# Optimization experiments

Measured on AMD Instinct MI355X. Metric: run time of the kernel, lower is better.

Reference implementation:

```python
import jax, jax.numpy as jnp
import numpy as np

H = 4        # no_heads
C = 32       # c_hidden per head
CQ = 128     # c_q = c_k = c_v
N = 256      # pair dim / seq len
B = 1


def setup_inputs() -> dict:
    key = jax.random.key(0)
    ks = jax.random.split(key, 8)
    q_x = jax.random.normal(ks[0], (B, N, N, CQ), dtype=jnp.float32)
    kv_x = jax.random.normal(ks[1], (B, N, N, CQ), dtype=jnp.float32)
    mask_bias = jnp.zeros((B, N, 1, 1, N), dtype=jnp.float32)
    pair_bias = jax.random.normal(ks[2], (B, 1, H, N, N), dtype=jnp.float32)
    s = 1.0 / np.sqrt(CQ)
    w_q = jax.random.normal(ks[3], (H * C, CQ), dtype=jnp.float32) * s
    w_k = jax.random.normal(ks[4], (H * C, CQ), dtype=jnp.float32) * s
    w_v = jax.random.normal(ks[5], (H * C, CQ), dtype=jnp.float32) * s
    w_g = jax.random.normal(ks[6], (H * C, CQ), dtype=jnp.float32) * s
    w_o = jax.random.normal(ks[7], (CQ, H * C), dtype=jnp.float32) * s
    return {"q_x": q_x, "kv_x": kv_x, "mask_bias": mask_bias,
            "pair_bias": pair_bias, "w_q": w_q, "w_k": w_k, "w_v": w_v,
            "w_g": w_g, "w_o": w_o}


def reference(q_x, kv_x, mask_bias, pair_bias, w_q, w_k, w_v, w_g, w_o):
    # project: [B, N, Q, c] -> [B, N, H, Q, C]
    def proj(x, w):
        y = jnp.einsum('...qc,dc->...qd', x, w)            # [B,N,Q,H*C]
        y = y.reshape(*y.shape[:-1], H, C)                 # [B,N,Q,H,C]
        return jnp.swapaxes(y, -2, -3)                     # [B,N,H,Q,C]

    q = proj(q_x, w_q) / jnp.sqrt(jnp.asarray(C, q_x.dtype))
    k = proj(kv_x, w_k)
    v = proj(kv_x, w_v)

    # scores [B, N, H, Q, K] with both biases added pre-softmax
    a = jnp.einsum('...hqd,...hkd->...hqk', q, k) + mask_bias + pair_bias
    a = jax.nn.softmax(a, axis=-1)
    o = jnp.einsum('...hqk,...hkd->...hqd', a, v)          # [B,N,H,Q,C]
    o = jnp.swapaxes(o, -2, -3)                            # [B,N,Q,H,C]
    o = o.reshape(*o.shape[:-2], H * C)                    # [B,N,Q,H*C]

    g = jax.nn.sigmoid(jnp.einsum('...qc,dc->...qd', q_x, w_g))
    o = o * g
    return jnp.einsum('...qd,cd->...qc', o, w_o)           # [B,N,Q,c_q]
```

## Files before the change

### kernel.cpp

```cpp
#include <hip/hip_runtime.h>
#include <hip/hip_bf16.h>

#define H 4
#define C 32
#define CQ 128
#define NSEQ 256
#define HC 128

typedef __bf16 bf16;
typedef __bf16 bf16x8 __attribute__((ext_vector_type(8)));
typedef __bf16 bf16x4 __attribute__((ext_vector_type(4)));
typedef float f32x4 __attribute__((ext_vector_type(4)));

#define MFMA16(a, b, c) __builtin_amdgcn_mfma_f32_16x16x32_bf16(a, b, c, 0, 0, 0)

#define LOG2E 1.4426950408889634f

__global__ __launch_bounds__(256) void prep_weights(const float* __restrict__ wq,
                                                    const float* __restrict__ wk,
                                                    const float* __restrict__ wv,
                                                    const float* __restrict__ wg,
                                                    const float* __restrict__ wo,
                                                    bf16* __restrict__ dst) {
    const int m = blockIdx.y;
    const float* src = (m == 0) ? wq : (m == 1) ? wk : (m == 2) ? wv : (m == 3) ? wg : wo;
    int i = blockIdx.x * 256 + threadIdx.x;
    float4 v = ((const float4*)src)[i];
    bf16x4 b = {(bf16)v.x, (bf16)v.y, (bf16)v.z, (bf16)v.w};
    ((bf16x4*)(dst + (size_t)m * 16384))[i] = b;
}

__global__ __launch_bounds__(256) void proj_all(const float* __restrict__ qx,
                                                const float* __restrict__ kvx,
                                                const bf16* __restrict__ wbf,
                                                bf16* __restrict__ qo,
                                                bf16* __restrict__ go,
                                                bf16* __restrict__ ko,
                                                bf16* __restrict__ vo) {
    __shared__ bf16 w1s[128][136];
    __shared__ bf16 w2s[128][136];

    const int t = threadIdx.x;
    const int mode = blockIdx.y;

    const float* x = mode ? kvx : qx;
    const bf16* w1 = wbf + (mode ? 1 : 0) * 16384;
    const bf16* w2 = wbf + (mode ? 2 : 3) * 16384;
    bf16* o1 = mode ? ko : qo;
    bf16* o2 = mode ? vo : go;

    #pragma unroll
    for (int i = t; i < 2048; i += 256) {
        int row = i >> 4, col = (i & 15) * 8;
        *(bf16x8*)&w1s[row][col] = *(const bf16x8*)&w1[row * CQ + col];
        *(bf16x8*)&w2s[row][col] = *(const bf16x8*)&w2[row * CQ + col];
    }
    __syncthreads();

    const int w = t >> 6, l = t & 63, lr = l & 15, lg = l >> 4;
    const float qscale = 0.17677669529663687f * LOG2E;

    for (int it = 0; it < 4; it++) {
        const int row0 = blockIdx.x * 256 + it * 64 + w * 16;

        bf16x8 a[4];
        #pragma unroll
        for (int ks = 0; ks < 4; ks++) {
            const float* p = x + (size_t)(row0 + lr) * CQ + ks * 32 + lg * 8;
            float4 lo = *(const float4*)p;
            float4 hi = *(const float4*)(p + 4);
            a[ks] = (bf16x8){(bf16)lo.x, (bf16)lo.y, (bf16)lo.z, (bf16)lo.w,
                             (bf16)hi.x, (bf16)hi.y, (bf16)hi.z, (bf16)hi.w};
        }

        f32x4 acc1[8], acc2[8];
        #pragma unroll
        for (int nt = 0; nt < 8; nt++) { acc1[nt] = (f32x4)0.f; acc2[nt] = (f32x4)0.f; }

        #pragma unroll
        for (int nt = 0; nt < 8; nt++) {
            #pragma unroll
            for (int ks = 0; ks < 4; ks++) {
                bf16x8 b1 = *(const bf16x8*)&w1s[nt * 16 + lr][ks * 32 + lg * 8];
                acc1[nt] = MFMA16(a[ks], b1, acc1[nt]);
            }
            #pragma unroll
            for (int ks = 0; ks < 4; ks++) {
                bf16x8 b2 = *(const bf16x8*)&w2s[nt * 16 + lr][ks * 32 + lg * 8];
                acc2[nt] = MFMA16(a[ks], b2, acc2[nt]);
            }
        }

        #pragma unroll
        for (int nt = 0; nt < 8; nt++) {
            #pragma unroll
            for (int r = 0; r < 4; r++) {
                const int row = row0 + lg * 4 + r;
                const int col = nt * 16 + lr;
                float v1 = acc1[nt][r], v2 = acc2[nt][r];
                if (mode == 0) {
                    v1 *= qscale;
                    v2 = __builtin_amdgcn_rcpf(1.f + __builtin_amdgcn_exp2f(-v2 * LOG2E));
                }
                o1[(size_t)row * HC + col] = (bf16)v1;
                o2[(size_t)row * HC + col] = (bf16)v2;
            }
        }
    }
}

__global__ __launch_bounds__(256) void attn_kernel(const bf16* __restrict__ qw,
                                                   const bf16* __restrict__ kw,
                                                   const bf16* __restrict__ vw,
                                                   const bf16* __restrict__ gw,
                                                   const float* __restrict__ pair_bias,
                                                   const float* __restrict__ mask_bias,
                                                   bf16* __restrict__ ow) {
    const int wg = blockIdx.x;
    const int swz = ((wg & 7) << 9) + (wg >> 3);
    const int qc = swz & 3;
    const int n1 = (swz >> 2) & 255;
    const int h = swz >> 10;

    __shared__ bf16 klds[256][40];
    __shared__ bf16 vts[32][256];
    __shared__ bf16 ps[4][16][132];

    const int t = threadIdx.x;

    {
        const size_t base = ((size_t)n1 * NSEQ) * HC + (size_t)h * C;
        const int rr = t >> 2, cc4 = t & 3, ch = cc4 * 8;
        #pragma unroll
        for (int p = 0; p < 4; p++) {
            int row = p * 64 + rr;
            bf16x8 kv = *(const bf16x8*)&kw[base + (size_t)row * HC + ch];
            *(bf16x8*)&klds[row][ch] = kv;
            bf16x8 vv = *(const bf16x8*)&vw[base + (size_t)row * HC + ch];
            #pragma unroll
            for (int j = 0; j < 8; j++) {
                int colw = row ^ (cc4 << 4) ^ (j << 3);
                vts[ch + j][colw] = vv[j];
            }
        }
    }

    const int w = t >> 6, l = t & 63, lr = l & 15, lg = l >> 4;
    const int qbase = qc * 64 + w * 16;

    bf16x8 qf = *(const bf16x8*)&qw[((size_t)(n1 * NSEQ + qbase + lr)) * HC + h * C + lg * 8];

    const float* pb = pair_bias + (size_t)h * NSEQ * NSEQ;
    const float* mb = mask_bias + (size_t)n1 * NSEQ;

    __syncthreads();

    f32x4 s[16];
    #pragma unroll
    for (int kt = 0; kt < 16; kt++) {
        float mbk = mb[kt * 16 + lr] * LOG2E;
        #pragma unroll
        for (int r = 0; r < 4; r++)
            s[kt][r] = fmaf(pb[(size_t)(qbase + lg * 4 + r) * NSEQ + kt * 16 + lr],
                            LOG2E, mbk);
    }
    #pragma unroll
    for (int kt = 0; kt < 16; kt++) {
        bf16x8 kf = *(const bf16x8*)&klds[kt * 16 + lr][lg * 8];
        s[kt] = MFMA16(qf, kf, s[kt]);
    }

    float pinv[4];
    #pragma unroll
    for (int r = 0; r < 4; r++) {
        float mx = s[0][r];
        #pragma unroll
        for (int kt = 1; kt < 16; kt++) mx = fmaxf(mx, s[kt][r]);
        #pragma unroll
        for (int msk = 8; msk >= 1; msk >>= 1) mx = fmaxf(mx, __shfl_xor(mx, msk, 64));
        float sum = 0.f;
        #pragma unroll
        for (int kt = 0; kt < 16; kt++) {
            float e = __builtin_amdgcn_exp2f(s[kt][r] - mx);
            s[kt][r] = e;
            sum += e;
        }
        #pragma unroll
        for (int msk = 8; msk >= 1; msk >>= 1) sum += __shfl_xor(sum, msk, 64);
        pinv[r] = __builtin_amdgcn_rcpf(sum);
    }

    f32x4 o[2];
    o[0] = (f32x4)0.f;
    o[1] = (f32x4)0.f;
    #pragma unroll
    for (int hf = 0; hf < 2; hf++) {
        #pragma unroll
        for (int kt2 = 0; kt2 < 8; kt2++) {
            #pragma unroll
            for (int r = 0; r < 4; r++)
                ps[w][lg * 4 + r][kt2 * 16 + lr] = (bf16)(s[hf * 8 + kt2][r] * pinv[r]);
        }
        #pragma unroll
        for (int kh = 0; kh < 4; kh++) {
            bf16x8 pf = *(const bf16x8*)&ps[w][lr][kh * 32 + lg * 8];
            #pragma unroll
            for (int ct = 0; ct < 2; ct++) {
                int g2 = (2 * ct + (lr >> 3)) & 3;
                int col0 = (hf * 128 + kh * 32 + lg * 8) ^ (g2 << 4) ^ ((lr & 7) << 3);
                bf16x8 vf = *(const bf16x8*)&vts[ct * 16 + lr][col0];
                o[ct] = MFMA16(pf, vf, o[ct]);
            }
        }
    }

    #pragma unroll
    for (int ct = 0; ct < 2; ct++) {
        #pragma unroll
        for (int r = 0; r < 4; r++) {
            size_t idx = ((size_t)(n1 * NSEQ + qbase + lg * 4 + r)) * HC + (size_t)h * C +
                         ct * 16 + lr;
            float gv = (float)gw[idx];
            ow[idx] = (bf16)(o[ct][r] * gv);
        }
    }
}

__global__ __launch_bounds__(256) void out_proj(const bf16* __restrict__ og,
                                                const bf16* __restrict__ wo,
                                                float* __restrict__ out) {
    __shared__ bf16 ws[128][136];
    const int t = threadIdx.x;

    #pragma unroll
    for (int i = t; i < 2048; i += 256) {
        int row = i >> 4, col = (i & 15) * 8;
        *(bf16x8*)&ws[row][col] = *(const bf16x8*)&wo[row * CQ + col];
    }
    __syncthreads();

    const int w = t >> 6, l = t & 63, lr = l & 15, lg = l >> 4;

    for (int it = 0; it < 4; it++) {
        const int row0 = blockIdx.x * 256 + it * 64 + w * 16;

        bf16x8 a[4];
        #pragma unroll
        for (int ks = 0; ks < 4; ks++)
            a[ks] = *(const bf16x8*)&og[(size_t)(row0 + lr) * HC + ks * 32 + lg * 8];

        f32x4 acc[8];
        #pragma unroll
        for (int nt = 0; nt < 8; nt++) acc[nt] = (f32x4)0.f;
        #pragma unroll
        for (int nt = 0; nt < 8; nt++) {
            #pragma unroll
            for (int ks = 0; ks < 4; ks++) {
                bf16x8 b = *(const bf16x8*)&ws[nt * 16 + lr][ks * 32 + lg * 8];
                acc[nt] = MFMA16(a[ks], b, acc[nt]);
            }
        }

        #pragma unroll
        for (int nt = 0; nt < 8; nt++)
            #pragma unroll
            for (int r = 0; r < 4; r++)
                out[(size_t)(row0 + lg * 4 + r) * CQ + nt * 16 + lr] = acc[nt][r];
    }
}

extern "C" void kernel_launch(void* const* d_in, const int* in_sizes, int n_in,
                              void* d_out, int out_size, void* d_ws, size_t ws_size,
                              hipStream_t stream) {
    const float* q_x = (const float*)d_in[0];
    const float* kv_x = (const float*)d_in[1];
    const float* mask_bias = (const float*)d_in[2];
    const float* pair_bias = (const float*)d_in[3];
    const float* w_q = (const float*)d_in[4];
    const float* w_k = (const float*)d_in[5];
    const float* w_v = (const float*)d_in[6];
    const float* w_g = (const float*)d_in[7];
    const float* w_o = (const float*)d_in[8];

    const size_t M = (size_t)NSEQ * NSEQ;
    bf16* wbf = (bf16*)d_ws;
    bf16* qws = wbf + 5 * 16384;
    bf16* gws = qws + M * HC;
    bf16* kws = gws + M * HC;
    bf16* vws = kws + M * HC;
    bf16* ows = vws + M * HC;

    prep_weights<<<dim3(16, 5), 256, 0, stream>>>(w_q, w_k, w_v, w_g, w_o, wbf);
    proj_all<<<dim3(256, 2), 256, 0, stream>>>(q_x, kv_x, wbf, qws, gws, kws, vws);
    attn_kernel<<<dim3(4096), 256, 0, stream>>>(qws, kws, vws, gws, pair_bias,
                                                mask_bias, ows);
    out_proj<<<dim3(256), 256, 0, stream>>>(ows, wbf + 4 * 16384, (float*)d_out);
}
```

Baseline: 93.29 us.

## Swap MFMA operands so weights stay in registers and outputs store vectorized

The projection and output-projection kernels now use 512 threads. Each of the 8 waves holds a 16-column slice of the weight matrix in registers, and activations are the streamed B operand. The transposed MFMA output layout lets each lane write 4 contiguous outputs as one vector store instead of scattered scalar stores. The aim is to cut repeated LDS weight reads and uncoalesced global stores. The cost is that every wave reloads the same activation rows from global memory, and each wave does less MFMA work per load.

```diff
diff --git a/kernel.cpp b/kernel.cpp
--- a/kernel.cpp
+++ b/kernel.cpp
@@ -30,7 +30,7 @@
     ((bf16x4*)(dst + (size_t)m * 16384))[i] = b;
 }
 
-__global__ __launch_bounds__(256) void proj_all(const float* __restrict__ qx,
+__global__ __launch_bounds__(512) void proj_all(const float* __restrict__ qx,
                                                 const float* __restrict__ kvx,
                                                 const bf16* __restrict__ wbf,
                                                 bf16* __restrict__ qo,
@@ -50,62 +50,59 @@
     bf16* o2 = mode ? vo : go;
 
     #pragma unroll
-    for (int i = t; i < 2048; i += 256) {
+    for (int i = t; i < 2048; i += 512) {
         int row = i >> 4, col = (i & 15) * 8;
         *(bf16x8*)&w1s[row][col] = *(const bf16x8*)&w1[row * CQ + col];
         *(bf16x8*)&w2s[row][col] = *(const bf16x8*)&w2[row * CQ + col];
     }
     __syncthreads();
 
-    const int w = t >> 6, l = t & 63, lr = l & 15, lg = l >> 4;
+    const int w = t >> 6;
+    const int l = t & 63, lr = l & 15, lg = l >> 4;
+
+    bf16x8 a1[4], a2[4];
+    #pragma unroll
+    for (int ks = 0; ks < 4; ks++) {
+        a1[ks] = *(const bf16x8*)&w1s[w * 16 + lr][ks * 32 + lg * 8];
+        a2[ks] = *(const bf16x8*)&w2s[w * 16 + lr][ks * 32 + lg * 8];
+    }
+
     const float qscale = 0.17677669529663687f * LOG2E;
 
-    for (int it = 0; it < 4; it++) {
-        const int row0 = blockIdx.x * 256 + it * 64 + w * 16;
-
-        bf16x8 a[4];
+    for (int it = 0; it < 16; it++) {
+        const int row0 = blockIdx.x * 256 + it * 16;
+
+        bf16x8 b[4];
         #pragma unroll
         for (int ks = 0; ks < 4; ks++) {
             const float* p = x + (size_t)(row0 + lr) * CQ + ks * 32 + lg * 8;
             float4 lo = *(const float4*)p;
             float4 hi = *(const float4*)(p + 4);
-            a[ks] = (bf16x8){(bf16)lo.x, (bf16)lo.y, (bf16)lo.z, (bf16)lo.w,
+            b[ks] = (bf16x8){(bf16)lo.x, (bf16)lo.y, (bf16)lo.z, (bf16)lo.w,
                              (bf16)hi.x, (bf16)hi.y, (bf16)hi.z, (bf16)hi.w};
         }
 
-        f32x4 acc1[8], acc2[8];
-        #pragma unroll
-        for (int nt = 0; nt < 8; nt++) { acc1[nt] = (f32x4)0.f; acc2[nt] = (f32x4)0.f; }
-
-        #pragma unroll
-        for (int nt = 0; nt < 8; nt++) {
-            #pragma unroll
-            for (int ks = 0; ks < 4; ks++) {
-                bf16x8 b1 = *(const bf16x8*)&w1s[nt * 16 + lr][ks * 32 + lg * 8];
-                acc1[nt] = MFMA16(a[ks], b1, acc1[nt]);
+        f32x4 acc1 = (f32x4)0.f, acc2 = (f32x4)0.f;
+        #pragma unroll
+        for (int ks = 0; ks < 4; ks++) {
+            acc1 = MFMA16(a1[ks], b[ks], acc1);
+            acc2 = MFMA16(a2[ks], b[ks], acc2);
+        }
+
+        bf16x4 st1, st2;
+        #pragma unroll
+        for (int r = 0; r < 4; r++) {
+            float v1 = acc1[r], v2 = acc2[r];
+            if (mode == 0) {
+                v1 *= qscale;
+                v2 = __builtin_amdgcn_rcpf(1.f + __builtin_amdgcn_exp2f(-v2 * LOG2E));
             }
-            #pragma unroll
-            for (int ks = 0; ks < 4; ks++) {
-                bf16x8 b2 = *(const bf16x8*)&w2s[nt * 16 + lr][ks * 32 + lg * 8];
-                acc2[nt] = MFMA16(a[ks], b2, acc2[nt]);
-            }
-        }
-
-        #pragma unroll
-        for (int nt = 0; nt < 8; nt++) {
-            #pragma unroll
-            for (int r = 0; r < 4; r++) {
-                const int row = row0 + lg * 4 + r;
-                const int col = nt * 16 + lr;
-                float v1 = acc1[nt][r], v2 = acc2[nt][r];
-                if (mode == 0) {
-                    v1 *= qscale;
-                    v2 = __builtin_amdgcn_rcpf(1.f + __builtin_amdgcn_exp2f(-v2 * LOG2E));
-                }
-                o1[(size_t)row * HC + col] = (bf16)v1;
-                o2[(size_t)row * HC + col] = (bf16)v2;
-            }
-        }
+            st1[r] = (bf16)v1;
+            st2[r] = (bf16)v2;
+        }
+        const size_t obase = (size_t)(row0 + lr) * HC + w * 16 + lg * 4;
+        *(bf16x4*)&o1[obase] = st1;
+        *(bf16x4*)&o2[obase] = st2;
     }
 }
 
@@ -226,14 +223,14 @@
     }
 }
 
-__global__ __launch_bounds__(256) void out_proj(const bf16* __restrict__ og,
+__global__ __launch_bounds__(512) void out_proj(const bf16* __restrict__ og,
                                                 const bf16* __restrict__ wo,
                                                 float* __restrict__ out) {
     __shared__ bf16 ws[128][136];
     const int t = threadIdx.x;
 
     #pragma unroll
-    for (int i = t; i < 2048; i += 256) {
+    for (int i = t; i < 2048; i += 512) {
         int row = i >> 4, col = (i & 15) * 8;
         *(bf16x8*)&ws[row][col] = *(const bf16x8*)&wo[row * CQ + col];
     }
@@ -241,31 +238,26 @@
 
     const int w = t >> 6, l = t & 63, lr = l & 15, lg = l >> 4;
 
-    for (int it = 0; it < 4; it++) {
-        const int row0 = blockIdx.x * 256 + it * 64 + w * 16;
-
-        bf16x8 a[4];
+    bf16x8 a[4];
+    #pragma unroll
+    for (int ks = 0; ks < 4; ks++)
+        a[ks] = *(const bf16x8*)&ws[w * 16 + lr][ks * 32 + lg * 8];
+
+    for (int it = 0; it < 8; it++) {
+        const int row0 = blockIdx.x * 128 + it * 16;
+
+        bf16x8 b[4];
         #pragma unroll
         for (int ks = 0; ks < 4; ks++)
-            a[ks] = *(const bf16x8*)&og[(size_t)(row0 + lr) * HC + ks * 32 + lg * 8];
-
-        f32x4 acc[8];
-        #pragma unroll
-        for (int nt = 0; nt < 8; nt++) acc[nt] = (f32x4)0.f;
-        #pragma unroll
-        for (int nt = 0; nt < 8; nt++) {
-            #pragma unroll
-            for (int ks = 0; ks < 4; ks++) {
-                bf16x8 b = *(const bf16x8*)&ws[nt * 16 + lr][ks * 32 + lg * 8];
-                acc[nt] = MFMA16(a[ks], b, acc[nt]);
-            }
-        }
-
-        #pragma unroll
-        for (int nt = 0; nt < 8; nt++)
-            #pragma unroll
-            for (int r = 0; r < 4; r++)
-                out[(size_t)(row0 + lg * 4 + r) * CQ + nt * 16 + lr] = acc[nt][r];
+            b[ks] = *(const bf16x8*)&og[(size_t)(row0 + lr) * HC + ks * 32 + lg * 8];
+
+        f32x4 acc = (f32x4)0.f;
+        #pragma unroll
+        for (int ks = 0; ks < 4; ks++)
+            acc = MFMA16(a[ks], b[ks], acc);
+
+        *(float4*)&out[(size_t)(row0 + lr) * CQ + w * 16 + lg * 4] =
+            (float4){acc[0], acc[1], acc[2], acc[3]};
     }
 }
 
@@ -291,8 +283,8 @@
     bf16* ows = vws + M * HC;
 
     prep_weights<<<dim3(16, 5), 256, 0, stream>>>(w_q, w_k, w_v, w_g, w_o, wbf);
-    proj_all<<<dim3(256, 2), 256, 0, stream>>>(q_x, kv_x, wbf, qws, gws, kws, vws);
+    proj_all<<<dim3(256, 2), 512, 0, stream>>>(q_x, kv_x, wbf, qws, gws, kws, vws);
     attn_kernel<<<dim3(4096), 256, 0, stream>>>(qws, kws, vws, gws, pair_bias,
                                                 mask_bias, ows);
-    out_proj<<<dim3(256), 256, 0, stream>>>(ows, wbf + 4 * 16384, (float*)d_out);
-}
+    out_proj<<<dim3(512), 512, 0, stream>>>(ows, wbf + 4 * 16384, (float*)d_out);
+}
```

New measurement: 132.2 us. 41.7% more time.
